# Kernel tuning notes

Measured on AMD Instinct MI355X. Metric: run time of the kernel, lower is better.

Reference implementation:

```python
import jax, jax.numpy as jnp
import numpy as np

N_BITS = 8
IN_FEATURES = 2048
OUT_FEATURES = 512
BATCH = 8
THRESHOLD = 0.5


def setup_inputs() -> dict:
    key = jax.random.key(0)
    kx, kw = jax.random.split(key)
    x = jax.random.uniform(kx, (BATCH, IN_FEATURES), dtype=jnp.float32)
    # nn.init.normal_(weight, mean=0.5, std=1.0) then clamp_(0, 1)
    weight = 0.5 + jax.random.normal(kw, (IN_FEATURES, OUT_FEATURES * N_BITS), dtype=jnp.float32)
    weight = jnp.clip(weight, 0.0, 1.0)
    return {"x": x, "weight": weight}


def _carry_save_adder(addends):
    # addends: [M, F, n_bits] -> reduce over F via full-adder chain.
    # Bit index 0 = LSB; carry shifts one position toward MSB each step.
    M, F, nb = addends.shape
    a_seq = jnp.transpose(addends, (1, 0, 2))  # [F, M, nb]
    init = (jnp.zeros((M, nb), addends.dtype), jnp.zeros((M, nb), addends.dtype))

    def step(state, a):
        s, c = state
        t = s + a + c
        half = jnp.floor(t * 0.5)          # carry bit (zero-gradient)
        sum_b = t - 2.0 * half             # t mod 2 (identity gradient w.r.t. t)
        c_next = jnp.pad(half[:, :-1], ((0, 0), (1, 0)))  # shift-left: LSB carry-in = 0
        return (sum_b, c_next), None

    (s, c), _ = jax.lax.scan(step, init, a_seq)
    return s, c


def reference(x, weight):
    # STE binarization of the weights (forward value = hard bits)
    w = jnp.clip(weight, 0.0, 1.0)
    hard = w + jax.lax.stop_gradient((w >= THRESHOLD).astype(w.dtype) - w)
    # [B, F, 1] * [1, F, O*nb] -> [B, F, O*nb]
    ff = x[:, :, None] * hard[None, :, :]
    B, F, _ = ff.shape
    O = ff.shape[-1] // N_BITS
    # split(n_bits, dim=-1) + stack(dim=-3) + reshape -> [B*O, F, n_bits]
    stacked = ff.reshape(B, F, O, N_BITS).transpose(0, 2, 1, 3).reshape(B * O, F, N_BITS)
    s, carry = _carry_save_adder(stacked)   # [B*O, nb], [B*O, nb]
    s = s.reshape(B, N_BITS * O)
    return (s, carry)
```

## Files before the change

kernel.cpp:

```cpp
#include <hip/hip_runtime.h>


#define F_DIM 2048
#define K_DIM 4096
#define B_DIM 8
#define G     32
#define NG    (F_DIM / G)
#define NB2   4

#define PK_BYTES (64 * NG * 64 * 4)

__device__ __forceinline__ float dpp_row_shr1(float v) {
    int r = __builtin_amdgcn_update_dpp(0, __float_as_int(v), 0x111, 0xf, 0xf, true);
    return __int_as_float(r);
}

__device__ __forceinline__ int sext_bit(unsigned bits, int u) {
#if __has_builtin(__builtin_amdgcn_sbfe)
    return __builtin_amdgcn_sbfe((int)bits, (unsigned)u, 1u);
#else
    return ((int)(bits << (31 - u))) >> 31;
#endif
}

__global__ __launch_bounds__(64) void pack_kernel(const float* __restrict__ w,
                                                  unsigned* __restrict__ pk) {
    const int t   = threadIdx.x;
    const int ogq = blockIdx.x;
    const int f32 = blockIdx.y;

    const float4* w4 = (const float4*)(w + ogq * 256) + t;

    unsigned b0 = 0, b1 = 0, b2 = 0, b3 = 0;
#pragma unroll
    for (int j = 0; j < 32; ++j) {
        float4 v = w4[(f32 * 32 + j) * (K_DIM / 4)];
        b0 |= (v.x >= 0.5f ? 1u : 0u) << j;
        b1 |= (v.y >= 0.5f ? 1u : 0u) << j;
        b2 |= (v.z >= 0.5f ? 1u : 0u) << j;
        b3 |= (v.w >= 0.5f ? 1u : 0u) << j;
    }
    const int og  = ogq * 4 + (t >> 4);
    const int col = (t & 15) * 4;
    uint4* dst = (uint4*)(pk + (og * NG + f32) * 64 + col);
    *dst = make_uint4(b0, b1, b2, b3);
}

__global__ __launch_bounds__(64, 1) void csa_main(const float* __restrict__ x,
                                                  const unsigned* __restrict__ pk,
                                                  float* __restrict__ out) {
    const int lane = threadIdx.x;
    const int og   = blockIdx.x + 8 * blockIdx.y;
    const int b    = blockIdx.z;
    const int k    = og * 64 + lane;

    const float lsbmask = ((lane & 7) == 0) ? 0.0f : 1.0f;

    int zero;
    asm volatile("v_mov_b32 %0, 0" : "=v"(zero));

    const unsigned* bp  = pk + og * (NG * 64) + lane;
    const float4*   xp4 = (const float4*)(x + b * F_DIM) + zero;

    unsigned bbuf[NB2];
    float4   xb[NB2][G / 4];

#pragma unroll
    for (int p = 0; p < NB2; ++p) {
        bbuf[p] = bp[p * 64];
#pragma unroll
        for (int q = 0; q < G / 4; ++q)
            xb[p][q] = xp4[p * (G / 4) + q];
    }

    float s = 0.0f, craw = 0.0f;

    for (int g0 = 0; g0 < NG; g0 += NB2) {
#pragma unroll
        for (int p = 0; p < NB2; ++p) {
            const float*   xf   = (const float*)&xb[p][0];
            const unsigned bits = bbuf[p];
#pragma unroll
            for (int u = 0; u < G; ++u) {
                int   m  = sext_bit(bits, u);
                float a  = __int_as_float(m & __float_as_int(xf[u]));
                float uu = s + a;
                float t  = fmaf(craw, lsbmask, uu);
                float h  = floorf(t * 0.5f);
                s = fmaf(-2.0f, h, t);
                craw = dpp_row_shr1(h);
            }
            int gb = g0 + p + NB2;
            int gc = (gb < NG) ? gb : (NG - 1);
            bbuf[p] = bp[gc * 64];
#pragma unroll
            for (int q = 0; q < G / 4; ++q)
                xb[p][q] = xp4[gc * (G / 4) + q];
        }
    }

    out[b * K_DIM + k]                 = s;
    out[B_DIM * K_DIM + b * K_DIM + k] = craw * lsbmask;
}

#define U_FB  16
#define NB_FB 4
__global__ __launch_bounds__(64, 1) void csa_fallback(const float* __restrict__ x,
                                                      const float* __restrict__ weight,
                                                      float* __restrict__ out) {
    const int lane = threadIdx.x;
    const int og   = blockIdx.x + 8 * blockIdx.y;
    const int b    = blockIdx.z;
    const int k    = og * 64 + lane;
    const float lsbmask = ((lane & 7) == 0) ? 0.0f : 1.0f;
    int zero;
    asm volatile("v_mov_b32 %0, 0" : "=v"(zero));
    const float*  wp  = weight + k;
    const float4* xp4 = (const float4*)(x + b * F_DIM) + zero;
    float  wb[NB_FB][U_FB];
    float4 xb[NB_FB][U_FB / 4];
#pragma unroll
    for (int p = 0; p < NB_FB; ++p) {
#pragma unroll
        for (int u = 0; u < U_FB; ++u) wb[p][u] = wp[(p * U_FB + u) * K_DIM];
#pragma unroll
        for (int q = 0; q < U_FB / 4; ++q) xb[p][q] = xp4[(p * U_FB) / 4 + q];
    }
    float s = 0.0f, craw = 0.0f;
    for (int f0 = 0; f0 < F_DIM; f0 += NB_FB * U_FB) {
#pragma unroll
        for (int p = 0; p < NB_FB; ++p) {
            const float* xf = (const float*)&xb[p][0];
#pragma unroll
            for (int u = 0; u < U_FB; ++u) {
                float a  = (wb[p][u] >= 0.5f) ? xf[u] : 0.0f;
                float uu = s + a;
                float t  = fmaf(craw, lsbmask, uu);
                float h  = floorf(t * 0.5f);
                s = fmaf(-2.0f, h, t);
                craw = dpp_row_shr1(h);
            }
            int fb = f0 + p * U_FB + NB_FB * U_FB;
            int fc = (fb <= F_DIM - U_FB) ? fb : (F_DIM - U_FB);
#pragma unroll
            for (int u = 0; u < U_FB; ++u) wb[p][u] = wp[(fc + u) * K_DIM];
#pragma unroll
            for (int q = 0; q < U_FB / 4; ++q) xb[p][q] = xp4[fc / 4 + q];
        }
    }
    out[b * K_DIM + k]                 = s;
    out[B_DIM * K_DIM + b * K_DIM + k] = craw * lsbmask;
}

extern "C" void kernel_launch(void* const* d_in, const int* in_sizes, int n_in,
                              void* d_out, int out_size, void* d_ws, size_t ws_size,
                              hipStream_t stream) {
    (void)in_sizes; (void)n_in; (void)out_size;
    const float* x      = (const float*)d_in[0];
    const float* weight = (const float*)d_in[1];
    float* out          = (float*)d_out;

    if (ws_size >= (size_t)PK_BYTES && d_ws != nullptr) {
        unsigned* pk = (unsigned*)d_ws;
        pack_kernel<<<dim3(16, 64, 1), dim3(64), 0, stream>>>(weight, pk);
        csa_main<<<dim3(8, 8, 8), dim3(64), 0, stream>>>(x, pk, out);
    } else {
        csa_fallback<<<dim3(8, 8, 8), dim3(64), 0, stream>>>(x, weight, out);
    }
}
```

Before: 124.8 us.

## Process two bit columns per lane with interleaved even/odd carry chains

Each lane now owns an even and an odd bit position of one output group, running two independent carry-save chains whose work interleaves to hide the serial floor/dpp dependency latency. The carry from odd to even bits within a lane passes through a register, and only the odd-bit carry crosses lanes via DPP. The packed-weight layout is changed to f32-major so each lane reads a uint2 per group. The grid shrinks to 256 single-wave blocks, and the prefetch depth drops from 4 to 2 groups. This gives more instruction-level parallelism per lane at the cost of half as many waves in flight.

```diff
diff --git a/kernel.cpp b/kernel.cpp
--- a/kernel.cpp
+++ b/kernel.cpp
@@ -6,9 +6,9 @@
 #define B_DIM 8
 #define G     32
 #define NG    (F_DIM / G)
-#define NB2   4
+#define NBX   2
 
-#define PK_BYTES (64 * NG * 64 * 4)
+#define PK_BYTES (NG * K_DIM * 4)
 
 __device__ __forceinline__ float dpp_row_shr1(float v) {
     int r = __builtin_amdgcn_update_dpp(0, __float_as_int(v), 0x111, 0xf, 0xf, true);
@@ -40,9 +40,7 @@
         b2 |= (v.z >= 0.5f ? 1u : 0u) << j;
         b3 |= (v.w >= 0.5f ? 1u : 0u) << j;
     }
-    const int og  = ogq * 4 + (t >> 4);
-    const int col = (t & 15) * 4;
-    uint4* dst = (uint4*)(pk + (og * NG + f32) * 64 + col);
+    uint4* dst = (uint4*)(pk + f32 * K_DIM + ogq * 256 + t * 4);
     *dst = make_uint4(b0, b1, b2, b3);
 }
 
@@ -50,57 +48,72 @@
                                                   const unsigned* __restrict__ pk,
                                                   float* __restrict__ out) {
     const int lane = threadIdx.x;
-    const int og   = blockIdx.x + 8 * blockIdx.y;
-    const int b    = blockIdx.z;
-    const int k    = og * 64 + lane;
+    const int og16 = blockIdx.x;
+    const int b    = blockIdx.y;
+    const int q    = lane & 3;
+    const int col  = og16 * 128 + (lane >> 2) * 8 + q * 2;
 
-    const float lsbmask = ((lane & 7) == 0) ? 0.0f : 1.0f;
+    const float qmask = (q == 0) ? 0.0f : 1.0f;
 
     int zero;
     asm volatile("v_mov_b32 %0, 0" : "=v"(zero));
 
-    const unsigned* bp  = pk + og * (NG * 64) + lane;
+    const unsigned* pkc = pk + col;
     const float4*   xp4 = (const float4*)(x + b * F_DIM) + zero;
 
-    unsigned bbuf[NB2];
-    float4   xb[NB2][G / 4];
+    uint2  bb[NBX];
+    float4 xb[NBX][G / 4];
 
 #pragma unroll
-    for (int p = 0; p < NB2; ++p) {
-        bbuf[p] = bp[p * 64];
+    for (int p = 0; p < NBX; ++p) {
+        bb[p] = *(const uint2*)(pkc + p * K_DIM);
 #pragma unroll
-        for (int q = 0; q < G / 4; ++q)
-            xb[p][q] = xp4[p * (G / 4) + q];
+        for (int qq = 0; qq < G / 4; ++qq)
+            xb[p][qq] = xp4[p * (G / 4) + qq];
     }
 
-    float s = 0.0f, craw = 0.0f;
+    float s_e = 0.0f, s_o = 0.0f;
+    float he  = 0.0f;
+    float craw = 0.0f;
 
-    for (int g0 = 0; g0 < NG; g0 += NB2) {
+    for (int g0 = 0; g0 < NG; g0 += NBX) {
 #pragma unroll
-        for (int p = 0; p < NB2; ++p) {
-            const float*   xf   = (const float*)&xb[p][0];
-            const unsigned bits = bbuf[p];
+        for (int p = 0; p < NBX; ++p) {
+            const float*   xf = (const float*)&xb[p][0];
+            const unsigned be = bb[p].x;
+            const unsigned bo = bb[p].y;
 #pragma unroll
             for (int u = 0; u < G; ++u) {
-                int   m  = sext_bit(bits, u);
-                float a  = __int_as_float(m & __float_as_int(xf[u]));
-                float uu = s + a;
-                float t  = fmaf(craw, lsbmask, uu);
-                float h  = floorf(t * 0.5f);
-                s = fmaf(-2.0f, h, t);
-                craw = dpp_row_shr1(h);
+                const int xbits = __float_as_int(xf[u]);
+                float a_o  = __int_as_float(sext_bit(bo, u) & xbits);
+                float u_o  = s_o + a_o;
+                float t_o  = u_o + he;
+                float hm_o = t_o * 0.5f;
+                float h_o  = __builtin_floorf(hm_o);
+                float craw_n = dpp_row_shr1(h_o);
+                float a_e  = __int_as_float(sext_bit(be, u) & xbits);
+                float u_e  = s_e + a_e;
+                float t_e  = __builtin_fmaf(craw, qmask, u_e);
+                float hm_e = t_e * 0.5f;
+                float h_e  = __builtin_floorf(hm_e);
+                s_o = __builtin_fmaf(-2.0f, h_o, t_o);
+                s_e = __builtin_fmaf(-2.0f, h_e, t_e);
+                he   = h_e;
+                craw = craw_n;
             }
-            int gb = g0 + p + NB2;
+            int gb = g0 + p + NBX;
             int gc = (gb < NG) ? gb : (NG - 1);
-            bbuf[p] = bp[gc * 64];
+            bb[p] = *(const uint2*)(pkc + gc * K_DIM);
 #pragma unroll
-            for (int q = 0; q < G / 4; ++q)
-                xb[p][q] = xp4[gc * (G / 4) + q];
+            for (int qq = 0; qq < G / 4; ++qq)
+                xb[p][qq] = xp4[gc * (G / 4) + qq];
         }
     }
 
-    out[b * K_DIM + k]                 = s;
-    out[B_DIM * K_DIM + b * K_DIM + k] = craw * lsbmask;
+    float2* so = (float2*)(out + b * K_DIM + col);
+    *so = make_float2(s_e, s_o);
+    float2* co = (float2*)(out + B_DIM * K_DIM + b * K_DIM + col);
+    *co = make_float2(craw * qmask, he);
 }
 
 #define U_FB  16
@@ -163,7 +176,7 @@
     if (ws_size >= (size_t)PK_BYTES && d_ws != nullptr) {
         unsigned* pk = (unsigned*)d_ws;
         pack_kernel<<<dim3(16, 64, 1), dim3(64), 0, stream>>>(weight, pk);
-        csa_main<<<dim3(8, 8, 8), dim3(64), 0, stream>>>(x, pk, out);
+        csa_main<<<dim3(32, 8, 1), dim3(64), 0, stream>>>(x, pk, out);
     } else {
         csa_fallback<<<dim3(8, 8, 8), dim3(64), 0, stream>>>(x, weight, out);
     }
```

After: 145.9 us. 16.9% more time.

## Skew carry-save chain per bit lane to take DPP shift off critical path

Applied to the files above, without the earlier changes.

Each bit position j now processes the input sequence delayed by j steps, using skewed pre-packed weight bits and a pre-shifted x buffer built by new kernels. Carries are consumed two steps after they are produced, so the cross-lane DPP shift no longer sits on the serial per-step dependency chain. An 8-step epilogue drains the skew and selects each lane's final carry. This adds a build_xs kernel, a larger workspace, and one extra group of iterations, and reduces prefetch depth from four buffers to two.

```diff
diff --git a/kernel.cpp b/kernel.cpp
--- a/kernel.cpp
+++ b/kernel.cpp
@@ -5,10 +5,14 @@
 #define K_DIM 4096
 #define B_DIM 8
 #define G     32
-#define NG    (F_DIM / G)
-#define NB2   4
-
-#define PK_BYTES (64 * NG * 64 * 4)
+#define NG    64
+#define NGS   65
+#define TROW  (NGS * G)
+
+#define PKS_BYTES (NGS * K_DIM * 4)
+#define XS_BYTES  (B_DIM * 8 * TROW * 4)
+#define WS_SKEW   (PKS_BYTES + XS_BYTES)
+#define PK5_BYTES (64 * NG * 64 * 4)
 
 __device__ __forceinline__ float dpp_row_shr1(float v) {
     int r = __builtin_amdgcn_update_dpp(0, __float_as_int(v), 0x111, 0xf, 0xf, true);
@@ -23,88 +27,185 @@
 #endif
 }
 
-__global__ __launch_bounds__(64) void pack_kernel(const float* __restrict__ w,
-                                                  unsigned* __restrict__ pk) {
-    const int t   = threadIdx.x;
-    const int ogq = blockIdx.x;
-    const int f32 = blockIdx.y;
-
-    const float4* w4 = (const float4*)(w + ogq * 256) + t;
-
+__global__ __launch_bounds__(64) void pack_pks(const float* __restrict__ w,
+                                               unsigned* __restrict__ pks) {
+    const int t    = threadIdx.x;
+    const int slab = blockIdx.x;
+    const int g    = blockIdx.y;
+    const int colbase = slab * 256 + t * 4;
+    const float4* w4 = (const float4*)(w + colbase);
+
+    const int j0 = (t * 4) & 7, j1 = (t * 4 + 1) & 7,
+              j2 = (t * 4 + 2) & 7, j3 = (t * 4 + 3) & 7;
     unsigned b0 = 0, b1 = 0, b2 = 0, b3 = 0;
 #pragma unroll
-    for (int j = 0; j < 32; ++j) {
-        float4 v = w4[(f32 * 32 + j) * (K_DIM / 4)];
-        b0 |= (v.x >= 0.5f ? 1u : 0u) << j;
-        b1 |= (v.y >= 0.5f ? 1u : 0u) << j;
-        b2 |= (v.z >= 0.5f ? 1u : 0u) << j;
-        b3 |= (v.w >= 0.5f ? 1u : 0u) << j;
-    }
-    const int og  = ogq * 4 + (t >> 4);
-    const int col = (t & 15) * 4;
-    uint4* dst = (uint4*)(pk + (og * NG + f32) * 64 + col);
+    for (int r0 = -7; r0 < 32; ++r0) {
+        int f = g * G + r0;
+        if (f >= 0 && f < F_DIM) {
+            float4 v = w4[f * (K_DIM / 4)];
+            unsigned u0 = (unsigned)(r0 + j0); if (u0 < 32u) b0 |= (v.x >= 0.5f ? 1u : 0u) << u0;
+            unsigned u1 = (unsigned)(r0 + j1); if (u1 < 32u) b1 |= (v.y >= 0.5f ? 1u : 0u) << u1;
+            unsigned u2 = (unsigned)(r0 + j2); if (u2 < 32u) b2 |= (v.z >= 0.5f ? 1u : 0u) << u2;
+            unsigned u3 = (unsigned)(r0 + j3); if (u3 < 32u) b3 |= (v.w >= 0.5f ? 1u : 0u) << u3;
+        }
+    }
+    uint4* dst = (uint4*)(pks + g * K_DIM + colbase);
     *dst = make_uint4(b0, b1, b2, b3);
 }
 
-__global__ __launch_bounds__(64, 1) void csa_main(const float* __restrict__ x,
-                                                  const unsigned* __restrict__ pk,
+__global__ __launch_bounds__(256) void build_xs(const float* __restrict__ x,
+                                                float* __restrict__ xs) {
+    const int row = blockIdx.x;
+    const int b = row >> 3, j = row & 7;
+    const float* xr = x + b * F_DIM;
+    float* dst = xs + row * TROW;
+    for (int tau = threadIdx.x; tau < TROW; tau += 256) {
+        int f = tau - j;
+        dst[tau] = (f >= 0 && f < F_DIM) ? xr[f] : 0.0f;
+    }
+}
+
+__global__ __launch_bounds__(64, 1) void csa_skew(const unsigned* __restrict__ pks,
+                                                  const float* __restrict__ xs,
                                                   float* __restrict__ out) {
     const int lane = threadIdx.x;
     const int og   = blockIdx.x + 8 * blockIdx.y;
     const int b    = blockIdx.z;
+    const int col  = og * 64 + lane;
+    const int j    = lane & 7;
+    const float lsbmask = (j == 0) ? 0.0f : 1.0f;
+
+    const unsigned* pc = pks + col;
+    const float4*   xr = (const float4*)(xs + (b * 8 + j) * TROW);
+
+    unsigned bb[2];
+    float4   xb[2][G / 4];
+#pragma unroll
+    for (int p = 0; p < 2; ++p) {
+        bb[p] = pc[p * K_DIM];
+#pragma unroll
+        for (int q = 0; q < G / 4; ++q)
+            xb[p][q] = xr[p * (G / 4) + q];
+    }
+
+    float s = 0.0f;
+    float craw1 = 0.0f;
+    float craw2 = 0.0f;
+
+    for (int g = 0; g < NG; g += 2) {
+#pragma unroll
+        for (int p = 0; p < 2; ++p) {
+            const float*   xf   = (const float*)&xb[p][0];
+            const unsigned bits = bb[p];
+#pragma unroll
+            for (int u = 0; u < G; ++u) {
+                float a  = __int_as_float(sext_bit(bits, u) & __float_as_int(xf[u]));
+                float uu = s + a;
+                float t  = __builtin_fmaf(craw2, lsbmask, uu);
+                float hm = t * 0.5f;
+                float h  = __builtin_floorf(hm);
+                s = __builtin_fmaf(-2.0f, h, t);
+                craw2 = craw1;
+                craw1 = dpp_row_shr1(h);
+            }
+            int gn = g + p + 2;
+            int gc = (gn < NGS) ? gn : (NGS - 1);
+            bb[p] = pc[gc * K_DIM];
+#pragma unroll
+            for (int q = 0; q < G / 4; ++q)
+                xb[p][q] = xr[gc * (G / 4) + q];
+        }
+    }
+
+    const unsigned bits_e = bb[0];
+    const float*   xe     = (const float*)&xb[0][0];
+    float cfin = 0.0f;
+#pragma unroll
+    for (int e = 0; e < 8; ++e) {
+        float a  = __int_as_float(sext_bit(bits_e, e) & __float_as_int(xe[e]));
+        float uu = s + a;
+        float t  = __builtin_fmaf(craw2, lsbmask, uu);
+        float hm = t * 0.5f;
+        float h  = __builtin_floorf(hm);
+        float sn = __builtin_fmaf(-2.0f, h, t);
+        cfin = (j == e) ? craw2 * lsbmask : cfin;
+        s    = (j >  e) ? sn : s;
+        craw2 = craw1;
+        craw1 = dpp_row_shr1(h);
+    }
+
+    out[b * K_DIM + col]                 = s;
+    out[B_DIM * K_DIM + b * K_DIM + col] = cfin;
+}
+
+#define NBX5 4
+__global__ __launch_bounds__(64) void pack_r5(const float* __restrict__ w,
+                                              unsigned* __restrict__ pk) {
+    const int t   = threadIdx.x;
+    const int ogq = blockIdx.x;
+    const int f32 = blockIdx.y;
+    const float4* w4 = (const float4*)(w + ogq * 256) + t;
+    unsigned b0 = 0, b1 = 0, b2 = 0, b3 = 0;
+#pragma unroll
+    for (int jj = 0; jj < 32; ++jj) {
+        float4 v = w4[(f32 * 32 + jj) * (K_DIM / 4)];
+        b0 |= (v.x >= 0.5f ? 1u : 0u) << jj;
+        b1 |= (v.y >= 0.5f ? 1u : 0u) << jj;
+        b2 |= (v.z >= 0.5f ? 1u : 0u) << jj;
+        b3 |= (v.w >= 0.5f ? 1u : 0u) << jj;
+    }
+    const int og  = ogq * 4 + (t >> 4);
+    const int c4  = (t & 15) * 4;
+    uint4* dst = (uint4*)(pk + (og * NG + f32) * 64 + c4);
+    *dst = make_uint4(b0, b1, b2, b3);
+}
+
+__global__ __launch_bounds__(64, 1) void csa_r5(const float* __restrict__ x,
+                                                const unsigned* __restrict__ pk,
+                                                float* __restrict__ out) {
+    const int lane = threadIdx.x;
+    const int og   = blockIdx.x + 8 * blockIdx.y;
+    const int b    = blockIdx.z;
     const int k    = og * 64 + lane;
-
     const float lsbmask = ((lane & 7) == 0) ? 0.0f : 1.0f;
-
     int zero;
     asm volatile("v_mov_b32 %0, 0" : "=v"(zero));
-
     const unsigned* bp  = pk + og * (NG * 64) + lane;
     const float4*   xp4 = (const float4*)(x + b * F_DIM) + zero;
-
-    unsigned bbuf[NB2];
-    float4   xb[NB2][G / 4];
-
-#pragma unroll
-    for (int p = 0; p < NB2; ++p) {
+    unsigned bbuf[NBX5];
+    float4   xb[NBX5][G / 4];
+#pragma unroll
+    for (int p = 0; p < NBX5; ++p) {
         bbuf[p] = bp[p * 64];
 #pragma unroll
-        for (int q = 0; q < G / 4; ++q)
-            xb[p][q] = xp4[p * (G / 4) + q];
-    }
-
+        for (int q = 0; q < G / 4; ++q) xb[p][q] = xp4[p * (G / 4) + q];
+    }
     float s = 0.0f, craw = 0.0f;
-
-    for (int g0 = 0; g0 < NG; g0 += NB2) {
-#pragma unroll
-        for (int p = 0; p < NB2; ++p) {
+    for (int g0 = 0; g0 < NG; g0 += NBX5) {
+#pragma unroll
+        for (int p = 0; p < NBX5; ++p) {
             const float*   xf   = (const float*)&xb[p][0];
             const unsigned bits = bbuf[p];
 #pragma unroll
             for (int u = 0; u < G; ++u) {
-                int   m  = sext_bit(bits, u);
-                float a  = __int_as_float(m & __float_as_int(xf[u]));
+                float a  = __int_as_float(sext_bit(bits, u) & __float_as_int(xf[u]));
                 float uu = s + a;
-                float t  = fmaf(craw, lsbmask, uu);
-                float h  = floorf(t * 0.5f);
-                s = fmaf(-2.0f, h, t);
+                float t  = __builtin_fmaf(craw, lsbmask, uu);
+                float h  = __builtin_floorf(t * 0.5f);
+                s = __builtin_fmaf(-2.0f, h, t);
                 craw = dpp_row_shr1(h);
             }
-            int gb = g0 + p + NB2;
+            int gb = g0 + p + NBX5;
             int gc = (gb < NG) ? gb : (NG - 1);
             bbuf[p] = bp[gc * 64];
 #pragma unroll
-            for (int q = 0; q < G / 4; ++q)
-                xb[p][q] = xp4[gc * (G / 4) + q];
-        }
-    }
-
+            for (int q = 0; q < G / 4; ++q) xb[p][q] = xp4[gc * (G / 4) + q];
+        }
+    }
     out[b * K_DIM + k]                 = s;
     out[B_DIM * K_DIM + b * K_DIM + k] = craw * lsbmask;
 }
 
-#define U_FB  16
-#define NB_FB 4
 __global__ __launch_bounds__(64, 1) void csa_fallback(const float* __restrict__ x,
                                                       const float* __restrict__ weight,
                                                       float* __restrict__ out) {
@@ -117,35 +218,35 @@
     asm volatile("v_mov_b32 %0, 0" : "=v"(zero));
     const float*  wp  = weight + k;
     const float4* xp4 = (const float4*)(x + b * F_DIM) + zero;
-    float  wb[NB_FB][U_FB];
-    float4 xb[NB_FB][U_FB / 4];
-#pragma unroll
-    for (int p = 0; p < NB_FB; ++p) {
-#pragma unroll
-        for (int u = 0; u < U_FB; ++u) wb[p][u] = wp[(p * U_FB + u) * K_DIM];
-#pragma unroll
-        for (int q = 0; q < U_FB / 4; ++q) xb[p][q] = xp4[(p * U_FB) / 4 + q];
+    float  wb[4][16];
+    float4 xb[4][4];
+#pragma unroll
+    for (int p = 0; p < 4; ++p) {
+#pragma unroll
+        for (int u = 0; u < 16; ++u) wb[p][u] = wp[(p * 16 + u) * K_DIM];
+#pragma unroll
+        for (int q = 0; q < 4; ++q) xb[p][q] = xp4[p * 4 + q];
     }
     float s = 0.0f, craw = 0.0f;
-    for (int f0 = 0; f0 < F_DIM; f0 += NB_FB * U_FB) {
-#pragma unroll
-        for (int p = 0; p < NB_FB; ++p) {
+    for (int f0 = 0; f0 < F_DIM; f0 += 64) {
+#pragma unroll
+        for (int p = 0; p < 4; ++p) {
             const float* xf = (const float*)&xb[p][0];
 #pragma unroll
-            for (int u = 0; u < U_FB; ++u) {
+            for (int u = 0; u < 16; ++u) {
                 float a  = (wb[p][u] >= 0.5f) ? xf[u] : 0.0f;
                 float uu = s + a;
-                float t  = fmaf(craw, lsbmask, uu);
-                float h  = floorf(t * 0.5f);
-                s = fmaf(-2.0f, h, t);
+                float t  = __builtin_fmaf(craw, lsbmask, uu);
+                float h  = __builtin_floorf(t * 0.5f);
+                s = __builtin_fmaf(-2.0f, h, t);
                 craw = dpp_row_shr1(h);
             }
-            int fb = f0 + p * U_FB + NB_FB * U_FB;
-            int fc = (fb <= F_DIM - U_FB) ? fb : (F_DIM - U_FB);
-#pragma unroll
-            for (int u = 0; u < U_FB; ++u) wb[p][u] = wp[(fc + u) * K_DIM];
-#pragma unroll
-            for (int q = 0; q < U_FB / 4; ++q) xb[p][q] = xp4[fc / 4 + q];
+            int fb = f0 + p * 16 + 64;
+            int fc = (fb <= F_DIM - 16) ? fb : (F_DIM - 16);
+#pragma unroll
+            for (int u = 0; u < 16; ++u) wb[p][u] = wp[(fc + u) * K_DIM];
+#pragma unroll
+            for (int q = 0; q < 4; ++q) xb[p][q] = xp4[fc / 4 + q];
         }
     }
     out[b * K_DIM + k]                 = s;
@@ -160,10 +261,16 @@
     const float* weight = (const float*)d_in[1];
     float* out          = (float*)d_out;
 
-    if (ws_size >= (size_t)PK_BYTES && d_ws != nullptr) {
+    if (ws_size >= (size_t)WS_SKEW && d_ws != nullptr) {
+        unsigned* pks = (unsigned*)d_ws;
+        float*    xs  = (float*)((char*)d_ws + PKS_BYTES);
+        pack_pks<<<dim3(16, 65, 1), dim3(64), 0, stream>>>(weight, pks);
+        build_xs<<<dim3(64, 1, 1), dim3(256), 0, stream>>>(x, xs);
+        csa_skew<<<dim3(8, 8, 8), dim3(64), 0, stream>>>(pks, xs, out);
+    } else if (ws_size >= (size_t)PK5_BYTES && d_ws != nullptr) {
         unsigned* pk = (unsigned*)d_ws;
-        pack_kernel<<<dim3(16, 64, 1), dim3(64), 0, stream>>>(weight, pk);
-        csa_main<<<dim3(8, 8, 8), dim3(64), 0, stream>>>(x, pk, out);
+        pack_r5<<<dim3(16, 64, 1), dim3(64), 0, stream>>>(weight, pk);
+        csa_r5<<<dim3(8, 8, 8), dim3(64), 0, stream>>>(x, pk, out);
     } else {
         csa_fallback<<<dim3(8, 8, 8), dim3(64), 0, stream>>>(x, weight, out);
     }
```

New measurement: 156.5 us. 25.4% more time.
